# Performance work log

Hardware: AMD Instinct MI355X
Metric: run time of the kernel (lower is better)

Reference implementation:

```python
import jax, jax.numpy as jnp
import numpy as np

D = 1024      # feature_dim
H = 16        # heads
HD = D // H   # head_dim
B, N = 8, 1024
LN_EPS = 1e-5


def setup_inputs() -> dict:
    key = jax.random.key(0)
    ks = jax.random.split(key, 12)
    s = 0.02
    return {
        "x": jax.random.normal(ks[0], (B, N, D), jnp.float32),
        "Wq": jax.random.normal(ks[1], (D, D), jnp.float32) * s,
        "bq": jnp.zeros((D,), jnp.float32),
        "Wk": jax.random.normal(ks[2], (D, D), jnp.float32) * s,
        "bk": jnp.zeros((D,), jnp.float32),
        "Wv": jax.random.normal(ks[3], (D, D), jnp.float32) * s,
        "bv": jnp.zeros((D,), jnp.float32),
        "pair_bias": jnp.zeros((D, D), jnp.float32),  # init zeros as in torch
        "Wo": jax.random.normal(ks[4], (D, D), jnp.float32) * s,
        "bo": jnp.zeros((D,), jnp.float32),
        "gamma": jnp.ones((D,), jnp.float32),
        "beta": jnp.zeros((D,), jnp.float32),
    }


def reference(x, Wq, bq, Wk, bk, Wv, bv, pair_bias, Wo, bo, gamma, beta):
    b, n, d = x.shape
    residual = x
    # projections -> [b, h, n, hd]
    def split_heads(t):
        return t.reshape(b, n, H, HD).transpose(0, 2, 1, 3)
    q = split_heads(x @ Wq + bq)
    k = split_heads(x @ Wk + bk)
    v = split_heads(x @ Wv + bv)
    # scores + shared pairwise bias (same bias for every batch/head)
    scores = jnp.einsum('bhqd,bhkd->bhqk', q, k) / jnp.sqrt(jnp.float32(HD))
    scores = scores + pair_bias[:n, :n][None, None, :, :]
    attn = jax.nn.softmax(scores, axis=-1)
    # dropout in eval mode == identity
    out = jnp.einsum('bhqk,bhkd->bhqd', attn, v)
    out = out.transpose(0, 2, 1, 3).reshape(b, n, d)
    out = out @ Wo + bo
    out = residual + out
    # LayerNorm
    mu = jnp.mean(out, axis=-1, keepdims=True)
    var = jnp.var(out, axis=-1, keepdims=True)
    out = (out - mu) * jax.lax.rsqrt(var + LN_EPS) * gamma + beta
    return out, attn
```

## Files before the change

kernel.cpp:

```cpp
#include <hip/hip_runtime.h>
#include <hip/hip_bf16.h>
#include <stdint.h>
#include <stddef.h>

#define DI __device__ __forceinline__

typedef unsigned short u16;
typedef float f32x4 __attribute__((ext_vector_type(4)));
typedef short bf16x8 __attribute__((ext_vector_type(8)));
typedef u16 u16x4 __attribute__((ext_vector_type(4)));

constexpr int Mm = 8192;
constexpr int Dd = 1024;
constexpr float LOG2E = 1.44269504088896f;

DI u16 bf(float f) {
  __hip_bfloat16 h = __float2bfloat16(f);
  return *reinterpret_cast<u16*>(&h);
}

DI float b2f(short s) {
  union { float f; unsigned u; } v;
  v.u = ((unsigned)(unsigned short)s) << 16;
  return v.f;
}

DI f32x4 mfma16(bf16x8 a, bf16x8 b, f32x4 c) {
  return __builtin_amdgcn_mfma_f32_16x16x32_bf16(a, b, c, 0, 0, 0);
}

DI void gload16(const u16* g, u16* l) {
  __builtin_amdgcn_global_load_lds(
      (const __attribute__((address_space(1))) void*)(g),
      (__attribute__((address_space(3))) void*)(l), 16, 0, 0);
}

__global__ __launch_bounds__(256) void k_prep(const float* __restrict__ x,
                                              u16* __restrict__ xb,
                                              const float* __restrict__ pb,
                                              u16* __restrict__ pbb,
                                              const float* __restrict__ W0,
                                              const float* __restrict__ W1,
                                              const float* __restrict__ W2,
                                              const float* __restrict__ W3,
                                              u16* __restrict__ T0,
                                              u16* __restrict__ T1,
                                              u16* __restrict__ T2,
                                              u16* __restrict__ T3) {
  __shared__ float t[32][33];
  const int bid = blockIdx.x;
  const int tid = threadIdx.x;
  if (bid < 8192) {
    size_t i = (size_t)bid * 256 + tid;
    float4 v = *(const float4*)(x + i * 4);
    u16x4 r;
    r.x = bf(v.x); r.y = bf(v.y); r.z = bf(v.z); r.w = bf(v.w);
    *(u16x4*)(xb + i * 4) = r;
  } else if (bid < 9216) {
    size_t i = (size_t)(bid - 8192) * 256 + tid;
    float4 v = *(const float4*)(pb + i * 4);
    u16x4 r;
    r.x = bf(v.x * LOG2E); r.y = bf(v.y * LOG2E);
    r.z = bf(v.z * LOG2E); r.w = bf(v.w * LOG2E);
    *(u16x4*)(pbb + i * 4) = r;
  } else {
    const int tt = bid - 9216;
    const int z = tt >> 10;
    const int rem = tt & 1023;
    const float* W;
    u16* T;
    switch (z) {
      case 0: W = W0; T = T0; break;
      case 1: W = W1; T = T1; break;
      case 2: W = W2; T = T2; break;
      default: W = W3; T = T3; break;
    }
    const int bx = (rem & 31) * 32;
    const int by = (rem >> 5) * 32;
    const int tx = tid & 31, ty = tid >> 5;
#pragma unroll
    for (int i = 0; i < 4; ++i)
      t[ty + i * 8][tx] = W[(size_t)(bx + ty + i * 8) * 1024 + by + tx];
    __syncthreads();
#pragma unroll
    for (int i = 0; i < 4; ++i)
      T[(size_t)(by + ty + i * 8) * 1024 + bx + tx] = bf(t[tx][ty + i * 8]);
  }
}

__global__ __launch_bounds__(256) void k_gemm_qkv(const u16* __restrict__ A,
                                                  const u16* __restrict__ wqT,
                                                  const u16* __restrict__ wkT,
                                                  const u16* __restrict__ wvT,
                                                  const float* __restrict__ bq,
                                                  const float* __restrict__ bk,
                                                  const float* __restrict__ bv,
                                                  u16* __restrict__ qo,
                                                  u16* __restrict__ ko,
                                                  u16* __restrict__ vo) {
  __shared__ __align__(16) u16 smem[2 * 128 * 64];
  u16* As = smem;
  u16* Bs = smem + 128 * 64;
  const int mode = blockIdx.z;
  const u16* WT = mode == 0 ? wqT : (mode == 1 ? wkT : wvT);
  const float* bias = mode == 0 ? bq : (mode == 1 ? bk : bv);
  const int tid = threadIdx.x;
  const int lane = tid & 63;
  const int wave = tid >> 6;
  const int brow = blockIdx.y * 128;
  const int bcol = blockIdx.x * 128;
  const int wr = (wave >> 1) * 64;
  const int wc = (wave & 1) * 64;
  const int l15 = lane & 15, l4 = lane >> 4;

  f32x4 acc[4][4] = {};
  const int crow0 = tid >> 3;
  const int kpos = (tid & 7) * 8;

  for (int t = 0; t < 16; ++t) {
    const int k0 = t * 64;
#pragma unroll
    for (int r = 0; r < 4; ++r) {
      int crow = r * 32 + crow0;
      u16* ldsbase_a = As + ((r * 256 + wave * 64) << 3);
      u16* ldsbase_b = Bs + ((r * 256 + wave * 64) << 3);
      gload16(A + (size_t)(brow + crow) * 1024 + k0 + kpos, ldsbase_a);
      gload16(WT + (size_t)(bcol + crow) * 1024 + k0 + kpos, ldsbase_b);
    }
    __syncthreads();
#pragma unroll
    for (int kk = 0; kk < 2; ++kk) {
      bf16x8 af[4], bg[4];
      const int kb = kk * 32 + l4 * 8;
#pragma unroll
      for (int mt = 0; mt < 4; ++mt)
        af[mt] = *(const bf16x8*)(As + (wr + mt * 16 + l15) * 64 + kb);
#pragma unroll
      for (int nt = 0; nt < 4; ++nt)
        bg[nt] = *(const bf16x8*)(Bs + (wc + nt * 16 + l15) * 64 + kb);
#pragma unroll
      for (int mt = 0; mt < 4; ++mt)
#pragma unroll
        for (int nt = 0; nt < 4; ++nt)
          acc[mt][nt] = mfma16(af[mt], bg[nt], acc[mt][nt]);
    }
    __syncthreads();
  }

  if (mode == 2) {
#pragma unroll
    for (int nt = 0; nt < 4; ++nt) {
      int dl = wc + nt * 16 + l15;
      float bvv = bias[bcol + dl];
#pragma unroll
      for (int mt = 0; mt < 4; ++mt) {
        int s4 = wr + mt * 16 + l4 * 4;
        u16x4 pk;
        pk.x = bf(acc[mt][nt][0] + bvv);
        pk.y = bf(acc[mt][nt][1] + bvv);
        pk.z = bf(acc[mt][nt][2] + bvv);
        pk.w = bf(acc[mt][nt][3] + bvv);
        *(u16x4*)(smem + dl * 128 + (s4 ^ ((dl & 7) << 3))) = pk;
      }
    }
    __syncthreads();
    const int bb = brow >> 10;
    const int seq0 = brow & 1023;
    const int chunk = tid & 15;
#pragma unroll
    for (int p = 0; p < 8; ++p) {
      int dl = p * 16 + (tid >> 4);
      bf16x8 v = *(const bf16x8*)(smem + dl * 128 + ((chunk * 8) ^ ((dl & 7) << 3)));
      *(bf16x8*)(vo + ((size_t)bb * 1024 + bcol + dl) * 1024 + seq0 + chunk * 8) = v;
    }
    return;
  }

  u16* outp = mode == 0 ? qo : ko;
  const float scale = mode == 0 ? (0.125f * LOG2E) : 1.0f;
#pragma unroll
  for (int nt = 0; nt < 4; ++nt) {
    int gc = bcol + wc + nt * 16 + l15;
    float bvv = bias[gc];
#pragma unroll
    for (int mt = 0; mt < 4; ++mt) {
#pragma unroll
      for (int i = 0; i < 4; ++i) {
        int gm = brow + wr + mt * 16 + l4 * 4 + i;
        outp[(size_t)gm * 1024 + gc] = bf((acc[mt][nt][i] + bvv) * scale);
      }
    }
  }
}

__global__ __launch_bounds__(256) void k_gemm_o(const u16* __restrict__ A,
                                                const u16* __restrict__ WT,
                                                const float* __restrict__ bias,
                                                const float* __restrict__ resid,
                                                float* __restrict__ outp) {
  __shared__ __align__(16) u16 smem[2 * 128 * 64];
  u16* As = smem;
  u16* Bs = smem + 128 * 64;
  const int tid = threadIdx.x;
  const int lane = tid & 63;
  const int wave = tid >> 6;
  const int brow = blockIdx.y * 128;
  const int bcol = blockIdx.x * 128;
  const int wr = (wave >> 1) * 64;
  const int wc = (wave & 1) * 64;
  const int l15 = lane & 15, l4 = lane >> 4;

  f32x4 acc[4][4] = {};
  const int crow0 = tid >> 3;
  const int kpos = (tid & 7) * 8;

  for (int t = 0; t < 16; ++t) {
    const int k0 = t * 64;
#pragma unroll
    for (int r = 0; r < 4; ++r) {
      int crow = r * 32 + crow0;
      u16* ldsbase_a = As + ((r * 256 + wave * 64) << 3);
      u16* ldsbase_b = Bs + ((r * 256 + wave * 64) << 3);
      gload16(A + (size_t)(brow + crow) * 1024 + k0 + kpos, ldsbase_a);
      gload16(WT + (size_t)(bcol + crow) * 1024 + k0 + kpos, ldsbase_b);
    }
    __syncthreads();
#pragma unroll
    for (int kk = 0; kk < 2; ++kk) {
      bf16x8 af[4], bg[4];
      const int kb = kk * 32 + l4 * 8;
#pragma unroll
      for (int mt = 0; mt < 4; ++mt)
        af[mt] = *(const bf16x8*)(As + (wr + mt * 16 + l15) * 64 + kb);
#pragma unroll
      for (int nt = 0; nt < 4; ++nt)
        bg[nt] = *(const bf16x8*)(Bs + (wc + nt * 16 + l15) * 64 + kb);
#pragma unroll
      for (int mt = 0; mt < 4; ++mt)
#pragma unroll
        for (int nt = 0; nt < 4; ++nt)
          acc[mt][nt] = mfma16(af[mt], bg[nt], acc[mt][nt]);
    }
    __syncthreads();
  }

#pragma unroll
  for (int nt = 0; nt < 4; ++nt) {
    int gc = bcol + wc + nt * 16 + l15;
    float bvv = bias[gc];
#pragma unroll
    for (int mt = 0; mt < 4; ++mt) {
#pragma unroll
      for (int i = 0; i < 4; ++i) {
        int gm = brow + wr + mt * 16 + l4 * 4 + i;
        outp[(size_t)gm * 1024 + gc] =
            acc[mt][nt][i] + bvv + resid[(size_t)gm * 1024 + gc];
      }
    }
  }
}

__global__ __launch_bounds__(256, 3) void k_attn(const u16* __restrict__ q,
                                                 const u16* __restrict__ kk_,
                                                 const u16* __restrict__ vt,
                                                 const u16* __restrict__ pbb,
                                                 float* __restrict__ attn_out,
                                                 u16* __restrict__ aout) {
  __shared__ __align__(16) u16 sc[16 * 1024];
  __shared__ __align__(16) u16 kst[4][2][1024];
  __shared__ float invbuf[16];
  const int tid = threadIdx.x;
  const int lane = tid & 63;
  const int wave = tid >> 6;
  const int bid = blockIdx.x;
  const int swz = (bid & 7) * 1024 + (bid >> 3);
  const int bh = swz >> 6;
  const int q0 = (swz & 63) * 16;
  const int b = bh >> 4, h = bh & 15;
  const int l15 = lane & 15, l4 = lane >> 4;
  const int srow8 = (lane >> 3) & 7;
  const int sgsw = (lane & 7) ^ srow8;
  u16* const kw = &kst[wave][0][0];
  const u16* vbase = vt + (size_t)(b * 1024 + h * 64 + wave * 16) * 1024 + sgsw * 8;

  bf16x8 qf0, qf1;
  {
    const u16* qp = q + ((size_t)(b * 1024 + q0 + l15)) * 1024 + h * 64 + l4 * 8;
    qf0 = *(const bf16x8*)qp;
    qf1 = *(const bf16x8*)(qp + 32);
  }

  {
    const int kvb = wave * 256;
    const u16* kbase = kk_ + (size_t)(b * 1024 + kvb) * 1024 + h * 64 + sgsw * 8;
    gload16(kbase + (size_t)srow8 * 1024, kw);
    gload16(kbase + (size_t)(8 + srow8) * 1024, kw + 512);
    for (int c = 0; c < 16; ++c) {
      if (c < 15) {
        const u16* nsrc = kbase + (size_t)((c + 1) * 16 + srow8) * 1024;
        u16* ndst = kw + ((c + 1) & 1) * 1024;
        gload16(nsrc, ndst);
        gload16(nsrc + 8 * 1024, ndst + 512);
        asm volatile("s_waitcnt vmcnt(2)" ::: "memory");
      } else {
        asm volatile("s_waitcnt vmcnt(0)" ::: "memory");
      }
      __builtin_amdgcn_sched_barrier(0);
      const u16* kb = kw + (c & 1) * 1024;
      const int r = l15;
      bf16x8 k0 = *(const bf16x8*)(kb + r * 64 + ((l4 ^ (r & 7)) << 3));
      bf16x8 k1 = *(const bf16x8*)(kb + r * 64 + (((4 + l4) ^ (r & 7)) << 3));
      f32x4 cc = {};
      cc = mfma16(k0, qf0, cc);
      cc = mfma16(k1, qf1, cc);
      const int c4 = kvb + c * 16 + l4 * 4;
      u16x4 pk;
      pk.x = bf(cc[0]); pk.y = bf(cc[1]); pk.z = bf(cc[2]); pk.w = bf(cc[3]);
      *(u16x4*)(sc + l15 * 1024 + (c4 ^ ((l15 & 7) << 3))) = pk;
    }
  }
  __syncthreads();

  gload16(vbase + (size_t)srow8 * 1024, kw);
  gload16(vbase + (size_t)(8 + srow8) * 1024, kw + 512);

  const int r2 = tid >> 4;
  const int l2 = tid & 15;
  {
    const int rx = (r2 & 7) << 3;
    u16* rowp = sc + r2 * 1024;
    const u16* pbrow = pbb + (size_t)(q0 + r2) * 1024 + l2 * 8;
    bf16x8 R[8];
#pragma unroll
    for (int g = 0; g < 8; ++g) {
      bf16x8 v = *(const bf16x8*)(rowp + ((g * 128 + l2 * 8) ^ rx));
      bf16x8 pv = *(const bf16x8*)(pbrow + g * 128);
      bf16x8 s;
#pragma unroll
      for (int j = 0; j < 8; ++j) s[j] = (short)bf(b2f(v[j]) + b2f(pv[j]));
      R[g] = s;
    }
    float mx = -3e38f;
#pragma unroll
    for (int g = 0; g < 8; ++g)
#pragma unroll
      for (int j = 0; j < 8; ++j) mx = fmaxf(mx, b2f(R[g][j]));
#pragma unroll
    for (int o = 1; o < 16; o <<= 1) mx = fmaxf(mx, __shfl_xor(mx, o));
    float sum = 0.f;
#pragma unroll
    for (int g = 0; g < 8; ++g) {
      bf16x8 e;
#pragma unroll
      for (int j = 0; j < 8; ++j) {
        float t = exp2f(b2f(R[g][j]) - mx);
        sum += t;
        e[j] = (short)bf(t);
      }
      *(bf16x8*)(rowp + ((g * 128 + l2 * 8) ^ rx)) = e;
    }
#pragma unroll
    for (int o = 1; o < 16; o <<= 1) sum += __shfl_xor(sum, o);
    if (l2 == 0) invbuf[r2] = 1.f / sum;
  }
  __syncthreads();

  f32x4 oacc = {};
  {
    for (int c = 0; c < 16; ++c) {
      if (c < 15) {
        const u16* nsrc = vbase + (size_t)srow8 * 1024 + (c + 1) * 64;
        u16* ndst = kw + ((c + 1) & 1) * 1024;
        gload16(nsrc, ndst);
        gload16(nsrc + 8 * 1024, ndst + 512);
        asm volatile("s_waitcnt vmcnt(2)" ::: "memory");
      } else {
        asm volatile("s_waitcnt vmcnt(0)" ::: "memory");
      }
      __builtin_amdgcn_sched_barrier(0);
      const u16* vb = kw + (c & 1) * 1024;
      const int vr = l15;
#pragma unroll
      for (int ks = 0; ks < 2; ++ks) {
        const int gg = ks * 4 + l4;
        bf16x8 vf = *(const bf16x8*)(vb + vr * 64 + ((gg ^ (vr & 7)) << 3));
        const int e = c * 64 + ks * 32 + l4 * 8;
        bf16x8 pf = *(const bf16x8*)(sc + l15 * 1024 + (e ^ ((l15 & 7) << 3)));
        oacc = mfma16(pf, vf, oacc);
      }
    }
  }

#pragma unroll
  for (int i = 0; i < 4; ++i) {
    float iv = invbuf[l4 * 4 + i];
    aout[(size_t)(b * 1024 + q0 + l4 * 4 + i) * 1024 + h * 64 + wave * 16 + l15] =
        bf(oacc[i] * iv);
  }
#pragma unroll
  for (int it = 0; it < 16; ++it) {
    const int ebase = (tid * 4) ^ ((it & 7) << 3);
    u16x4 p = *(const u16x4*)(sc + it * 1024 + ebase);
    const float iv = invbuf[it];
    f32x4 w;
    w[0] = b2f((short)p.x) * iv;
    w[1] = b2f((short)p.y) * iv;
    w[2] = b2f((short)p.z) * iv;
    w[3] = b2f((short)p.w) * iv;
    __builtin_nontemporal_store(
        w, (f32x4*)(attn_out + ((size_t)bh * 1024 + q0 + it) * 1024 + tid * 4));
  }
}

__global__ __launch_bounds__(256) void k_ln(const float* __restrict__ y,
                                            const float* __restrict__ g,
                                            const float* __restrict__ be,
                                            float* __restrict__ o) {
  const int lane = threadIdx.x & 63;
  const int wave = threadIdx.x >> 6;
  size_t row = (size_t)blockIdx.x * 4 + wave;
  const float* yr = y + row * 1024;
  float4 v[4];
  float s = 0.f, sq = 0.f;
#pragma unroll
  for (int i = 0; i < 4; ++i) {
    v[i] = *(const float4*)(yr + i * 256 + lane * 4);
    s += v[i].x + v[i].y + v[i].z + v[i].w;
    sq += v[i].x * v[i].x + v[i].y * v[i].y + v[i].z * v[i].z + v[i].w * v[i].w;
  }
#pragma unroll
  for (int off = 1; off < 64; off <<= 1) {
    s += __shfl_xor(s, off);
    sq += __shfl_xor(sq, off);
  }
  float mu = s * (1.f / 1024.f);
  float var = sq * (1.f / 1024.f) - mu * mu;
  float rs = rsqrtf(fmaxf(var, 0.f) + 1e-5f);
  float* orow = o + row * 1024;
#pragma unroll
  for (int i = 0; i < 4; ++i) {
    int c = i * 256 + lane * 4;
    float4 gg = *(const float4*)(g + c);
    float4 bb = *(const float4*)(be + c);
    float4 rr;
    rr.x = (v[i].x - mu) * rs * gg.x + bb.x;
    rr.y = (v[i].y - mu) * rs * gg.y + bb.y;
    rr.z = (v[i].z - mu) * rs * gg.z + bb.z;
    rr.w = (v[i].w - mu) * rs * gg.w + bb.w;
    *(float4*)(orow + c) = rr;
  }
}

extern "C" void kernel_launch(void* const* d_in, const int* in_sizes, int n_in,
                              void* d_out, int out_size, void* d_ws, size_t ws_size,
                              hipStream_t stream) {
  const float* x = (const float*)d_in[0];
  const float* Wq = (const float*)d_in[1];
  const float* bq = (const float*)d_in[2];
  const float* Wk = (const float*)d_in[3];
  const float* bk = (const float*)d_in[4];
  const float* Wv = (const float*)d_in[5];
  const float* bv = (const float*)d_in[6];
  const float* pb = (const float*)d_in[7];
  const float* Wo = (const float*)d_in[8];
  const float* bo = (const float*)d_in[9];
  const float* gamma = (const float*)d_in[10];
  const float* beta = (const float*)d_in[11];

  char* ws = (char*)d_ws;
  u16* xb = (u16*)(ws);
  u16* aows = (u16*)(ws);
  u16* wqT = (u16*)(ws + (16u << 20));
  u16* wkT = (u16*)(ws + (18u << 20));
  u16* wvT = (u16*)(ws + (20u << 20));
  u16* woT = (u16*)(ws + (22u << 20));
  u16* qws = (u16*)(ws + (24u << 20));
  u16* kws = (u16*)(ws + (40u << 20));
  u16* vtws = (u16*)(ws + (56u << 20));
  float* yws = (float*)(ws + (72u << 20));
  u16* pbb = (u16*)(ws + (72u << 20));

  float* out_ln = (float*)d_out;
  float* out_attn = out_ln + (size_t)Mm * Dd;

  k_prep<<<13312, 256, 0, stream>>>(x, xb, pb, pbb, Wq, Wk, Wv, Wo,
                                    wqT, wkT, wvT, woT);
  k_gemm_qkv<<<dim3(8, 64, 3), 256, 0, stream>>>(xb, wqT, wkT, wvT,
                                                 bq, bk, bv, qws, kws, vtws);
  k_attn<<<8192, 256, 0, stream>>>(qws, kws, vtws, pbb, out_attn, aows);
  k_gemm_o<<<dim3(8, 64), 256, 0, stream>>>(aows, woT, bo, x, yws);
  k_ln<<<2048, 256, 0, stream>>>(yws, gamma, beta, out_ln);
}
```

Measured before the change: 312.2 us.

## Split attention waves into PV-matmul and attn-probability writer roles

After: 310.0 us. No clear change (-0.7%).

```diff
diff --git a/kernel.cpp b/kernel.cpp
--- a/kernel.cpp
+++ b/kernel.cpp
@@ -267,7 +267,7 @@
                                                  float* __restrict__ attn_out,
                                                  u16* __restrict__ aout) {
   __shared__ __align__(16) u16 sc[16 * 1024];
-  __shared__ __align__(16) u16 kst[4][2][1024];
+  __shared__ __align__(16) u16 kst[8192];
   __shared__ float invbuf[16];
   const int tid = threadIdx.x;
   const int lane = tid & 63;
@@ -280,8 +280,6 @@
   const int l15 = lane & 15, l4 = lane >> 4;
   const int srow8 = (lane >> 3) & 7;
   const int sgsw = (lane & 7) ^ srow8;
-  u16* const kw = &kst[wave][0][0];
-  const u16* vbase = vt + (size_t)(b * 1024 + h * 64 + wave * 16) * 1024 + sgsw * 8;
 
   bf16x8 qf0, qf1;
   {
@@ -291,6 +289,7 @@
   }
 
   {
+    u16* const kw = kst + wave * 2048;
     const int kvb = wave * 256;
     const u16* kbase = kk_ + (size_t)(b * 1024 + kvb) * 1024 + h * 64 + sgsw * 8;
     gload16(kbase + (size_t)srow8 * 1024, kw);
@@ -321,8 +320,13 @@
   }
   __syncthreads();
 
-  gload16(vbase + (size_t)srow8 * 1024, kw);
-  gload16(vbase + (size_t)(8 + srow8) * 1024, kw + 512);
+  const u16* vbase2 = vt + (size_t)(b * 1024 + h * 64 + wave * 32 + srow8) * 1024 + sgsw * 8;
+  u16* const kw3 = kst + wave * 4096;
+  if (wave < 2) {
+#pragma unroll
+    for (int i = 0; i < 4; ++i)
+      gload16(vbase2 + (size_t)(i * 8) * 1024, kw3 + i * 512);
+  }
 
   const int r2 = tid >> 4;
   const int l2 = tid & 15;
@@ -365,50 +369,59 @@
   }
   __syncthreads();
 
-  f32x4 oacc = {};
-  {
+  if (wave < 2) {
+    f32x4 oacc[2] = {};
     for (int c = 0; c < 16; ++c) {
       if (c < 15) {
-        const u16* nsrc = vbase + (size_t)srow8 * 1024 + (c + 1) * 64;
-        u16* ndst = kw + ((c + 1) & 1) * 1024;
-        gload16(nsrc, ndst);
-        gload16(nsrc + 8 * 1024, ndst + 512);
-        asm volatile("s_waitcnt vmcnt(2)" ::: "memory");
+        const u16* nsrc = vbase2 + (c + 1) * 64;
+        u16* ndst = kw3 + ((c + 1) & 1) * 2048;
+#pragma unroll
+        for (int i = 0; i < 4; ++i)
+          gload16(nsrc + (size_t)(i * 8) * 1024, ndst + i * 512);
+        asm volatile("s_waitcnt vmcnt(4)" ::: "memory");
       } else {
         asm volatile("s_waitcnt vmcnt(0)" ::: "memory");
       }
       __builtin_amdgcn_sched_barrier(0);
-      const u16* vb = kw + (c & 1) * 1024;
-      const int vr = l15;
+      const u16* vb = kw3 + (c & 1) * 2048;
 #pragma unroll
       for (int ks = 0; ks < 2; ++ks) {
         const int gg = ks * 4 + l4;
-        bf16x8 vf = *(const bf16x8*)(vb + vr * 64 + ((gg ^ (vr & 7)) << 3));
         const int e = c * 64 + ks * 32 + l4 * 8;
         bf16x8 pf = *(const bf16x8*)(sc + l15 * 1024 + (e ^ ((l15 & 7) << 3)));
-        oacc = mfma16(pf, vf, oacc);
-      }
-    }
-  }
-
-#pragma unroll
-  for (int i = 0; i < 4; ++i) {
-    float iv = invbuf[l4 * 4 + i];
-    aout[(size_t)(b * 1024 + q0 + l4 * 4 + i) * 1024 + h * 64 + wave * 16 + l15] =
-        bf(oacc[i] * iv);
-  }
-#pragma unroll
-  for (int it = 0; it < 16; ++it) {
-    const int ebase = (tid * 4) ^ ((it & 7) << 3);
-    u16x4 p = *(const u16x4*)(sc + it * 1024 + ebase);
-    const float iv = invbuf[it];
-    f32x4 w;
-    w[0] = b2f((short)p.x) * iv;
-    w[1] = b2f((short)p.y) * iv;
-    w[2] = b2f((short)p.z) * iv;
-    w[3] = b2f((short)p.w) * iv;
-    __builtin_nontemporal_store(
-        w, (f32x4*)(attn_out + ((size_t)bh * 1024 + q0 + it) * 1024 + tid * 4));
+#pragma unroll
+        for (int dg = 0; dg < 2; ++dg) {
+          const int vr = dg * 16 + l15;
+          bf16x8 vf = *(const bf16x8*)(vb + vr * 64 + ((gg ^ (vr & 7)) << 3));
+          oacc[dg] = mfma16(pf, vf, oacc[dg]);
+        }
+      }
+    }
+#pragma unroll
+    for (int dg = 0; dg < 2; ++dg)
+#pragma unroll
+      for (int i = 0; i < 4; ++i) {
+        float iv = invbuf[l4 * 4 + i];
+        aout[(size_t)(b * 1024 + q0 + l4 * 4 + i) * 1024 + h * 64 + wave * 32 +
+             dg * 16 + l15] = bf(oacc[dg][i] * iv);
+      }
+  } else {
+    const int tid2 = tid - 128;
+#pragma unroll
+    for (int it = 0; it < 32; ++it) {
+      const int row = it >> 1;
+      const int col4 = (it & 1) * 128 + tid2;
+      const int ebase = (col4 * 4) ^ ((row & 7) << 3);
+      u16x4 p = *(const u16x4*)(sc + row * 1024 + ebase);
+      const float iv = invbuf[row];
+      f32x4 w;
+      w[0] = b2f((short)p.x) * iv;
+      w[1] = b2f((short)p.y) * iv;
+      w[2] = b2f((short)p.z) * iv;
+      w[3] = b2f((short)p.w) * iv;
+      __builtin_nontemporal_store(
+          w, (f32x4*)(attn_out + ((size_t)bh * 1024 + q0 + row) * 1024 + col4 * 4));
+    }
   }
 }
 
```
